# Optimization experiments

Measured on AMD Instinct MI355X. Metric: run time of the kernel, lower is better.

Reference implementation:

```python
import jax, jax.numpy as jnp
import numpy as np

IN_DIM = 128
MEM_DIM = 256
NUM_CLASSES = 12
NUM_LEVELS = 17  # complete binary tree, N = 2**17 - 1 = 131071 nodes


def setup_inputs() -> dict:
    key = jax.random.key(0)
    ks = jax.random.split(key, 7)
    N = 2 ** NUM_LEVELS - 1
    s = 1.0 / np.sqrt(MEM_DIM)  # PyTorch LSTMCell/Linear init scale
    return {
        "x": jax.random.normal(ks[0], (N, IN_DIM), dtype=jnp.float32),
        "W_ih": jax.random.uniform(ks[1], (4 * MEM_DIM, IN_DIM), jnp.float32, -s, s),
        "b_ih": jax.random.uniform(ks[2], (4 * MEM_DIM,), jnp.float32, -s, s),
        "W_hh": jax.random.uniform(ks[3], (4 * MEM_DIM, MEM_DIM), jnp.float32, -s, s),
        "b_hh": jax.random.uniform(ks[4], (4 * MEM_DIM,), jnp.float32, -s, s),
        "W_fc": jax.random.uniform(ks[5], (NUM_CLASSES, MEM_DIM), jnp.float32, -s, s),
        "b_fc": jax.random.uniform(ks[6], (NUM_CLASSES,), jnp.float32, -s, s),
        "num_levels": NUM_LEVELS,
    }


def reference(x, W_ih, b_ih, W_hh, b_hh, W_fc, b_fc, num_levels):
    # Complete binary tree in BFS order: level l occupies nodes [2^l-1, 2^(l+1)-2];
    # children of level-l nodes are exactly the (contiguous) level-(l+1) nodes.
    mem = W_hh.shape[1]
    h_below = None
    c_below = None
    for l in reversed(range(num_levels)):
        n = 2 ** l
        x_l = x[n - 1:2 * n - 1]  # [n, in_dim] nodes at this level
        if h_below is None:  # leaves: zero child state
            ch_h = jnp.zeros((n, mem), dtype=x.dtype)
            ch_c = ch_h
        else:  # sum the two children's (h, c), as the recursion accumulates
            ch_h = h_below.reshape(n, 2, mem).sum(axis=1)
            ch_c = c_below.reshape(n, 2, mem).sum(axis=1)
        # PyTorch LSTMCell: gates = x W_ih^T + b_ih + h W_hh^T + b_hh, chunks i,f,g,o
        gates = x_l @ W_ih.T + b_ih + ch_h @ W_hh.T + b_hh  # [n, 4*mem]
        i, f, g, o = jnp.split(gates, 4, axis=-1)
        c_new = jax.nn.sigmoid(f) * ch_c + jax.nn.sigmoid(i) * jnp.tanh(g)
        h_new = jax.nn.sigmoid(o) * jnp.tanh(c_new)
        h_below, c_below = h_new, c_new
    # Original applies FC to state[1] == cell state c of the root (kept faithfully).
    return c_below[:1] @ W_fc.T + b_fc  # [1, num_classes]
```

## Files before the change

kernel.cpp:

```cpp
#include <hip/hip_runtime.h>
#include <hip/hip_bf16.h>
#include <cstddef>

#define IN_DIM 128
#define MEM 256
#define KTOT 384
#define NLEAF 65536
#define NBLK_TAIL 8

typedef float f32x4 __attribute__((ext_vector_type(4)));
typedef short s16x8 __attribute__((ext_vector_type(8)));
typedef unsigned int u32;

__device__ inline unsigned short f2bf(float f){
    unsigned int u = __builtin_bit_cast(unsigned int, f);
    u += 0x7fff + ((u >> 16) & 1);
    return (unsigned short)(u >> 16);
}

__device__ inline void gld_lds16(const void* g, void* l){
    __builtin_amdgcn_global_load_lds((const __attribute__((address_space(1))) u32*)g,
                                     (__attribute__((address_space(3))) u32*)l, 16, 0, 0);
}
__device__ inline void gld_lds16_dev(const void* g, void* l){
    __builtin_amdgcn_global_load_lds((const __attribute__((address_space(1))) u32*)g,
                                     (__attribute__((address_space(3))) u32*)l, 16, 0, 17);
}
__device__ inline void st16_dev(unsigned short* p, unsigned short v){
    unsigned int vv = v;
    asm volatile("global_store_short %0, %1, off sc0 sc1" :: "v"(p), "v"(vv) : "memory");
}
__device__ inline void st32_dev(float* p, float v){
    asm volatile("global_store_dword %0, %1, off sc0 sc1" :: "v"(p), "v"(v) : "memory");
}

__device__ inline float fsigm(float x){
    return __builtin_amdgcn_rcpf(1.f + __expf(-x));
}
__device__ inline float ftanh(float x){
    return 2.f * __builtin_amdgcn_rcpf(1.f + __expf(-2.f * x)) - 1.f;
}

__host__ __device__ inline size_t offA(int l){
    if (l == 16) return 0;
    return 8388608u + 384u * (65536u - (1u << (l + 1)));
}
#define ARENA_ELEMS 33554048u
#define ARENA_PAD   65536u

__device__ inline void grid_barrier_nf(unsigned* ctr, unsigned target){
    asm volatile("s_waitcnt vmcnt(0)" ::: "memory");
    __syncthreads();
    if (threadIdx.x == 0){
        __hip_atomic_fetch_add(ctr, 1u, __ATOMIC_RELAXED, __HIP_MEMORY_SCOPE_AGENT);
        while (__hip_atomic_load(ctr, __ATOMIC_RELAXED, __HIP_MEMORY_SCOPE_AGENT) < target)
            __builtin_amdgcn_s_sleep(2);
    }
    __syncthreads();
}

__global__ void pack_kernel(const float* __restrict__ x,
                            const float* __restrict__ W_ih, const float* __restrict__ b_ih,
                            const float* __restrict__ W_hh, const float* __restrict__ b_hh,
                            unsigned short* __restrict__ Wp, float* __restrict__ bp,
                            unsigned short* __restrict__ Aarena, unsigned* __restrict__ ctr){
    const int stride = gridDim.x * blockDim.x;
    const int tid0 = blockIdx.x * blockDim.x + threadIdx.x;
    if (tid0 == 0){ ctr[0] = 0; }

    for (int g = tid0; g < 1024 * 48; g += stride){
        int row = g / 48, ko = (g - row * 48) * 8;
        const float* s = (ko < IN_DIM) ? (W_ih + (size_t)row * IN_DIM + ko)
                                       : (W_hh + (size_t)row * MEM + (ko - IN_DIM));
        f32x4 v0 = *(const f32x4*)s, v1 = *(const f32x4*)(s + 4);
        s16x8 o;
        #pragma unroll
        for (int e = 0; e < 4; ++e){ o[e] = (short)f2bf(v0[e]); o[4+e] = (short)f2bf(v1[e]); }
        *(s16x8*)(Wp + (size_t)row * KTOT + ko) = o;
        if (ko == 0) bp[row] = b_ih[row] + b_hh[row];
    }

    const int TOTAL_G = 65536 * 16;
    for (int g = tid0; g < TOTAL_G; g += stride){
        int j  = g >> 4;
        int ko = (g & 15) * 8;
        const f32x4* s = (const f32x4*)(x + (size_t)(65535 + j) * IN_DIM + ko);
        f32x4 v0 = s[0], v1 = s[1];
        s16x8 o;
        #pragma unroll
        for (int e = 0; e < 4; ++e){ o[e] = (short)f2bf(v0[e]); o[4+e] = (short)f2bf(v1[e]); }
        *(s16x8*)(Aarena + (size_t)j * IN_DIM + ko) = o;
    }
}

template<int NK, bool PACKX>
__global__ __launch_bounds__(512, 1) void gemm_lstm8p_kernel(
    const unsigned short* __restrict__ A, int n,
    const unsigned short* __restrict__ Wp, const float* __restrict__ bp,
    const float* __restrict__ csum_in,
    unsigned short* __restrict__ A_next, float* __restrict__ csum_out,
    const float* __restrict__ xsrc, unsigned short* __restrict__ arena)
{
    __shared__ __align__(16) unsigned short As[2][2][128 * 64];
    __shared__ __align__(16) unsigned short Bs[2][2][128 * 64];

    const int tid  = threadIdx.x;
    const int lane = tid & 63;
    const int wid  = tid >> 6;
    const int wm   = wid >> 2;
    const int wn   = wid & 3;
    const int row0 = blockIdx.x * 256;
    const int m0   = blockIdx.y * 64;
    const int mg   = m0 + wn * 16 + (lane & 15);

    auto stageA = [&](int kt, int h){
        #pragma unroll
        for (int i = 0; i < 2; ++i){
            int p  = i * 512 + tid;
            int r  = p >> 3;
            int ls = (p & 7) ^ (r & 7);
            gld_lds16(A + (size_t)(row0 + h * 128 + r) * NK + kt * 64 + ls * 8,
                      (char*)As[kt & 1][h] + (size_t)(i * 512 + wid * 64) * 16);
        }
    };
    auto stageB = [&](int kt, int h){
        #pragma unroll
        for (int i = 0; i < 2; ++i){
            int p  = i * 512 + tid;
            int r  = p >> 3;
            int b  = h * 128 + r;
            int grow = (b >> 6) * 256 + m0 + (b & 63);
            int ls = (p & 7) ^ (r & 7);
            gld_lds16(Wp + (size_t)grow * KTOT + kt * 64 + ls * 8,
                      (char*)Bs[kt & 1][h] + (size_t)(i * 512 + wid * 64) * 16);
        }
    };

    f32x4 acc[8][4];
    #pragma unroll
    for (int r = 0; r < 8; ++r)
        #pragma unroll
        for (int q = 0; q < 4; ++q)
            acc[r][q] = (f32x4){0.f, 0.f, 0.f, 0.f};

    constexpr int nkt = NK / 64;
    stageA(0, 0); stageA(0, 1); stageB(0, 0);
    if (nkt > 1) stageB(1, 0);
    stageB(0, 1);

    s16x8 bfr[2][2];

    #pragma unroll
    for (int t = 0; t < nkt; ++t){
        const unsigned short* Ab = As[t & 1][wm];
        const unsigned short* Bb0 = Bs[t & 1][0];
        const unsigned short* Bb1 = Bs[t & 1][1];

        if (t + 1 < nkt) { asm volatile("s_waitcnt vmcnt(4)" ::: "memory"); }
        else             { asm volatile("s_waitcnt vmcnt(2)" ::: "memory"); }
        __builtin_amdgcn_s_barrier();
        asm volatile("" ::: "memory");

        #pragma unroll
        for (int rh = 0; rh < 2; ++rh){
            s16x8 a[4][2];
            #pragma unroll
            for (int j = 0; j < 4; ++j)
                #pragma unroll
                for (int ks = 0; ks < 2; ++ks){
                    int kb = (((ks * 4 + (lane >> 4)) ^ (lane & 7))) * 8;
                    a[j][ks] = *(const s16x8*)(Ab + (size_t)(rh * 64 + j * 16 + (lane & 15)) * 64 + kb);
                }
            if (rh == 0){
                #pragma unroll
                for (int q2 = 0; q2 < 2; ++q2)
                    #pragma unroll
                    for (int ks = 0; ks < 2; ++ks){
                        int kb = (((ks * 4 + (lane >> 4)) ^ (lane & 7))) * 8;
                        bfr[q2][ks] = *(const s16x8*)(Bb0 + (size_t)(q2 * 64 + wn * 16 + (lane & 15)) * 64 + kb);
                    }
                if (t + 1 < nkt) stageA(t + 1, 0);
            } else {
                if (t + 1 < nkt) stageA(t + 1, 1);
            }
            __builtin_amdgcn_s_setprio(1);
            #pragma unroll
            for (int j = 0; j < 4; ++j)
                #pragma unroll
                for (int q2 = 0; q2 < 2; ++q2)
                    #pragma unroll
                    for (int ks = 0; ks < 2; ++ks)
                        acc[rh * 4 + j][q2] = __builtin_amdgcn_mfma_f32_16x16x32_bf16(
                            a[j][ks], bfr[q2][ks], acc[rh * 4 + j][q2], 0, 0, 0);
            __builtin_amdgcn_s_setprio(0);
        }

        if (t + 1 < nkt) { asm volatile("s_waitcnt vmcnt(4)" ::: "memory"); }
        else             { asm volatile("s_waitcnt vmcnt(0)" ::: "memory"); }
        __builtin_amdgcn_s_barrier();
        asm volatile("" ::: "memory");

        #pragma unroll
        for (int rh = 0; rh < 2; ++rh){
            s16x8 a[4][2];
            #pragma unroll
            for (int j = 0; j < 4; ++j)
                #pragma unroll
                for (int ks = 0; ks < 2; ++ks){
                    int kb = (((ks * 4 + (lane >> 4)) ^ (lane & 7))) * 8;
                    a[j][ks] = *(const s16x8*)(Ab + (size_t)(rh * 64 + j * 16 + (lane & 15)) * 64 + kb);
                }
            if (rh == 0){
                #pragma unroll
                for (int q2 = 0; q2 < 2; ++q2)
                    #pragma unroll
                    for (int ks = 0; ks < 2; ++ks){
                        int kb = (((ks * 4 + (lane >> 4)) ^ (lane & 7))) * 8;
                        bfr[q2][ks] = *(const s16x8*)(Bb1 + (size_t)(q2 * 64 + wn * 16 + (lane & 15)) * 64 + kb);
                    }
                if (t + 2 < nkt) stageB(t + 2, 0);
            } else {
                if (t + 1 < nkt) stageB(t + 1, 1);
            }
            __builtin_amdgcn_s_setprio(1);
            #pragma unroll
            for (int j = 0; j < 4; ++j)
                #pragma unroll
                for (int q2 = 0; q2 < 2; ++q2)
                    #pragma unroll
                    for (int ks = 0; ks < 2; ++ks)
                        acc[rh * 4 + j][2 + q2] = __builtin_amdgcn_mfma_f32_16x16x32_bf16(
                            a[j][ks], bfr[q2][ks], acc[rh * 4 + j][2 + q2], 0, 0, 0);
            __builtin_amdgcn_s_setprio(0);
        }
        __builtin_amdgcn_s_barrier();
        asm volatile("" ::: "memory");
    }

    const float b0 = bp[0 * 256 + mg];
    const float b1 = bp[1 * 256 + mg];
    const float b2 = bp[2 * 256 + mg];
    const float b3 = bp[3 * 256 + mg];
    #pragma unroll
    for (int r = 0; r < 8; ++r){
        const int base = row0 + wm * 128 + r * 16 + (lane >> 4) * 4;
        float cpre[4];
        #pragma unroll
        for (int e = 0; e < 4; ++e)
            cpre[e] = csum_in[(size_t)(base + e) * MEM + mg];
        float cn[4], hn[4];
        #pragma unroll
        for (int e = 0; e < 4; ++e){
            float iv = acc[r][0][e] + b0;
            float fv = acc[r][1][e] + b1;
            float gv = acc[r][2][e] + b2;
            float ov = acc[r][3][e] + b3;
            float c  = fsigm(fv) * cpre[e] + fsigm(iv) * ftanh(gv);
            cn[e] = c;
            hn[e] = fsigm(ov) * ftanh(c);
        }
        int p0 = base >> 1;
        A_next[(size_t)p0 * KTOT + IN_DIM + mg] = f2bf(hn[0] + hn[1]);
        csum_out[(size_t)p0 * MEM + mg] = cn[0] + cn[1];
        A_next[(size_t)(p0 + 1) * KTOT + IN_DIM + mg] = f2bf(hn[2] + hn[3]);
        csum_out[(size_t)(p0 + 1) * MEM + mg] = cn[2] + cn[3];
    }

    if constexpr (PACKX){
        const int TG = 32767 * 16;
        const int bid = blockIdx.y * gridDim.x + blockIdx.x;
        const int stride_g = gridDim.x * gridDim.y * 512;
        for (int g = bid * 512 + tid; g < TG; g += stride_g){
            int i  = g >> 4;
            int ko = (g & 15) * 8;
            int l  = 31 - __clz(i + 1);
            int j  = i + 1 - (1 << l);
            size_t dst = offA(l) + (size_t)j * KTOT + ko;
            const f32x4* s = (const f32x4*)(xsrc + (size_t)i * IN_DIM + ko);
            f32x4 v0 = s[0], v1 = s[1];
            s16x8 o;
            #pragma unroll
            for (int e = 0; e < 4; ++e){ o[e] = (short)f2bf(v0[e]); o[4+e] = (short)f2bf(v1[e]); }
            *(s16x8*)(arena + dst) = o;
        }
    }
}

#define KC 64

template<int NK, int RB, bool LEAF, bool PACKX>
__global__ __launch_bounds__(256) void gemm_lstm_kernel(
    const unsigned short* __restrict__ A, int n,
    const unsigned short* __restrict__ Wp, const float* __restrict__ bp,
    const float* __restrict__ csum_in,
    unsigned short* __restrict__ A_next, float* __restrict__ csum_out,
    const float* __restrict__ xsrc, unsigned short* __restrict__ arena)
{
    constexpr int BM = RB * 32;
    __shared__ __align__(16) unsigned short As[2][BM * KC];
    __shared__ __align__(16) unsigned short Bs[2][128 * KC];

    const int tid  = threadIdx.x;
    const int lane = tid & 63;
    const int wid  = tid >> 6;
    const int wm   = wid >> 1;
    const int wc   = wid & 1;
    const int row0 = blockIdx.x * BM;
    const int m0   = blockIdx.y * 32;

    const int srow = lane >> 3;
    const int scol = ((lane & 7) ^ srow) * 8;

    const int mg = m0 + wc * 16 + (lane & 15);

    const float b0 = bp[0 * 256 + mg];
    const float b1 = LEAF ? 0.f : bp[1 * 256 + mg];
    const float b2 = bp[2 * 256 + mg];
    const float b3 = bp[3 * 256 + mg];
    float cpre[RB][4];
    if (!LEAF){
        #pragma unroll
        for (int r = 0; r < RB; ++r){
            const int base = row0 + wm * (RB * 16) + r * 16 + (lane >> 4) * 4;
            #pragma unroll
            for (int e = 0; e < 4; ++e)
                cpre[r][e] = csum_in[(size_t)(base + e) * MEM + mg];
        }
    }

    f32x4 acc[RB][4];
    #pragma unroll
    for (int r = 0; r < RB; ++r)
        #pragma unroll
        for (int q = 0; q < 4; ++q)
            acc[r][q] = (f32x4){0.f, 0.f, 0.f, 0.f};

    auto stage = [&](int d, int kk){
        char* asb = (char*)As[d];
        char* bsb = (char*)Bs[d];
        #pragma unroll
        for (int q = 0; q < RB; ++q){
            int t = wid * RB + q;
            int r = t * 8 + srow;
            gld_lds16(A + (size_t)(row0 + r) * NK + kk + scol, asb + t * 1024);
        }
        #pragma unroll
        for (int q = 0; q < 4; ++q){
            int t = wid * 4 + q;
            int b = t * 8 + srow;
            int grow = (b >> 5) * 256 + m0 + (b & 31);
            gld_lds16(Wp + (size_t)grow * KTOT + kk + scol, bsb + t * 1024);
        }
    };

    constexpr int nIter = NK / KC;
    stage(0, 0);
    int buf = 0;
    #pragma unroll
    for (int it = 0; it < nIter; ++it){
        if (it + 1 < nIter){
            stage(buf ^ 1, (it + 1) * KC);
            if constexpr (RB == 4) asm volatile("s_waitcnt vmcnt(8)" ::: "memory");
            else                   asm volatile("s_waitcnt vmcnt(6)" ::: "memory");
        } else {
            asm volatile("s_waitcnt vmcnt(0)" ::: "memory");
        }
        __builtin_amdgcn_s_barrier();
        const unsigned short* Ab = As[buf];
        const unsigned short* Bb = Bs[buf];
        #pragma unroll
        for (int ks = 0; ks < 2; ++ks){
            const int slot = ks * 4 + (lane >> 4);
            const int kb = (slot ^ (lane & 7)) * 8;
            s16x8 a[RB], b[4];
            #pragma unroll
            for (int r = 0; r < RB; ++r)
                a[r] = *(const s16x8*)(Ab + (wm * (RB * 16) + r * 16 + (lane & 15)) * KC + kb);
            #pragma unroll
            for (int q = 0; q < 4; ++q)
                b[q] = *(const s16x8*)(Bb + (q * 32 + wc * 16 + (lane & 15)) * KC + kb);
            #pragma unroll
            for (int r = 0; r < RB; ++r)
                #pragma unroll
                for (int q = 0; q < 4; ++q)
                    acc[r][q] = __builtin_amdgcn_mfma_f32_16x16x32_bf16(a[r], b[q], acc[r][q], 0, 0, 0);
        }
        __builtin_amdgcn_s_barrier();
        buf ^= 1;
    }

    #pragma unroll
    for (int r = 0; r < RB; ++r){
        const int base = row0 + wm * (RB * 16) + r * 16 + (lane >> 4) * 4;
        float cn[4], hn[4];
        #pragma unroll
        for (int e = 0; e < 4; ++e){
            float iv = acc[r][0][e] + b0;
            float gv = acc[r][2][e] + b2;
            float ov = acc[r][3][e] + b3;
            float c;
            if (LEAF){
                c = fsigm(iv) * ftanh(gv);
            } else {
                float fv = acc[r][1][e] + b1;
                c = fsigm(fv) * cpre[r][e] + fsigm(iv) * ftanh(gv);
            }
            cn[e] = c;
            hn[e] = fsigm(ov) * ftanh(c);
        }
        if (base < n){
            int p0 = base >> 1;
            A_next[(size_t)p0 * KTOT + IN_DIM + mg] = f2bf(hn[0] + hn[1]);
            csum_out[(size_t)p0 * MEM + mg] = cn[0] + cn[1];
        }
        if (base + 2 < n){
            int p1 = (base >> 1) + 1;
            A_next[(size_t)p1 * KTOT + IN_DIM + mg] = f2bf(hn[2] + hn[3]);
            csum_out[(size_t)p1 * MEM + mg] = cn[2] + cn[3];
        }
    }

    if constexpr (PACKX){
        const int TG = 32768 * 16;
        const int bid = blockIdx.y * gridDim.x + blockIdx.x;
        const int stride_g = gridDim.x * gridDim.y * 256;
        for (int g = bid * 256 + tid; g < TG; g += stride_g){
            int i  = 32767 + (g >> 4);
            int ko = (g & 15) * 8;
            size_t dst = offA(15) + (size_t)(i - 32767) * KTOT + ko;
            const f32x4* s = (const f32x4*)(xsrc + (size_t)i * IN_DIM + ko);
            f32x4 v0 = s[0], v1 = s[1];
            s16x8 o;
            #pragma unroll
            for (int e = 0; e < 4; ++e){ o[e] = (short)f2bf(v0[e]); o[4+e] = (short)f2bf(v1[e]); }
            *(s16x8*)(arena + dst) = o;
        }
    }
}

__global__ __launch_bounds__(512) void tail_kernel(
    const unsigned short* __restrict__ arena,
    const unsigned short* __restrict__ Wp, const float* __restrict__ bp,
    float* cs_in, float* cs_out,
    float* __restrict__ c_root,
    const float* __restrict__ W_fc, const float* __restrict__ b_fc,
    float* __restrict__ out, unsigned* __restrict__ ctr)
{
    __shared__ __align__(16) unsigned short WpL[128 * KTOT];
    __shared__ __align__(16) unsigned short AL[64 * KTOT];

    const int tid  = threadIdx.x;
    const int lane = tid & 63;
    const int wid  = tid >> 6;
    const int wm   = wid >> 1;
    const int wc   = wid & 1;
    const int m0   = blockIdx.x * 32;
    const int mg   = m0 + wc * 16 + (lane & 15);

    #pragma unroll
    for (int i = 0; i < 12; ++i){
        int p0 = wid * 768 + i * 64;
        int p  = p0 + lane;
        int lrow  = p / 48;
        int pslot = p % 48;
        int lslot = pslot ^ (lrow & 7);
        int grow  = (lrow >> 5) * 256 + m0 + (lrow & 31);
        gld_lds16(Wp + (size_t)grow * KTOT + lslot * 8, (char*)WpL + (size_t)p0 * 16);
    }

    const float b0 = bp[0 * 256 + mg];
    const float b1 = bp[1 * 256 + mg];
    const float b2 = bp[2 * 256 + mg];
    const float b3 = bp[3 * 256 + mg];

    asm volatile("s_waitcnt vmcnt(0)" ::: "memory");
    __builtin_amdgcn_s_barrier();

    unsigned gen = 0;
    for (int l = 7; l >= 0; --l){
        const int n = 1 << l;
        const unsigned short* Al = arena + offA(l);
        const int nhalf = (n > 64) ? (n >> 6) : 1;

        for (int h = 0; h < nhalf; ++h){
            const int r0 = h * 64;
            const int rows = (n < 64) ? n : 64;

            const int nslots = rows * 48;
            for (int t = 0; t * 512 < nslots; ++t){
                int pbase = t * 512 + wid * 64;
                int p = pbase + lane;
                if (p < nslots){
                    int row   = p / 48;
                    int pslot = p - row * 48;
                    int lslot = pslot ^ (row & 7);
                    gld_lds16_dev(Al + (size_t)(r0 + row) * KTOT + lslot * 8,
                                  (char*)AL + (size_t)pbase * 16);
                }
            }

            const int base = r0 + wm * 16 + (lane >> 4) * 4;
            float cpre[4];
            #pragma unroll
            for (int e = 0; e < 4; ++e)
                cpre[e] = __hip_atomic_load(&cs_in[(size_t)(base + e) * MEM + mg],
                                            __ATOMIC_RELAXED, __HIP_MEMORY_SCOPE_AGENT);

            asm volatile("s_waitcnt vmcnt(0)" ::: "memory");
            __builtin_amdgcn_s_barrier();

            f32x4 acc[4];
            #pragma unroll
            for (int q = 0; q < 4; ++q)
                acc[q] = (f32x4){0.f, 0.f, 0.f, 0.f};

            #pragma unroll
            for (int kc = 0; kc < 12; ++kc){
                const int ls = kc * 4 + (lane >> 4);
                const int kb = (ls ^ (lane & 7)) * 8;
                s16x8 a = *(const s16x8*)(AL + (size_t)(wm * 16 + (lane & 15)) * KTOT + kb);
                s16x8 b[4];
                #pragma unroll
                for (int q = 0; q < 4; ++q)
                    b[q] = *(const s16x8*)(WpL + (q * 32 + wc * 16 + (lane & 15)) * KTOT + kb);
                #pragma unroll
                for (int q = 0; q < 4; ++q)
                    acc[q] = __builtin_amdgcn_mfma_f32_16x16x32_bf16(a, b[q], acc[q], 0, 0, 0);
            }

            {
                float cn[4], hn[4];
                #pragma unroll
                for (int e = 0; e < 4; ++e){
                    float iv = acc[0][e] + b0;
                    float fv = acc[1][e] + b1;
                    float gv = acc[2][e] + b2;
                    float ov = acc[3][e] + b3;
                    float c  = fsigm(fv) * cpre[e] + fsigm(iv) * ftanh(gv);
                    cn[e] = c;
                    hn[e] = fsigm(ov) * ftanh(c);
                }
                if (l == 0){
                    if (base == 0) st32_dev(&c_root[mg], cn[0]);
                } else {
                    unsigned short* A_next = (unsigned short*)arena + offA(l - 1);
                    if (base < n){
                        int p0 = base >> 1;
                        st16_dev(&A_next[(size_t)p0 * KTOT + IN_DIM + mg], f2bf(hn[0] + hn[1]));
                        st32_dev(&cs_out[(size_t)p0 * MEM + mg], cn[0] + cn[1]);
                    }
                    if (base + 2 < n){
                        int p1 = (base >> 1) + 1;
                        st16_dev(&A_next[(size_t)p1 * KTOT + IN_DIM + mg], f2bf(hn[2] + hn[3]));
                        st32_dev(&cs_out[(size_t)p1 * MEM + mg], cn[2] + cn[3]);
                    }
                }
            }
            __builtin_amdgcn_s_barrier();
        }

        float* t = cs_in; cs_in = cs_out; cs_out = t;
        ++gen;
        grid_barrier_nf(ctr, (unsigned)(NBLK_TAIL * gen));
    }

    if (blockIdx.x == 0 && wid < 4){
        int w = wid;
        for (int cls = w * 3; cls < w * 3 + 3; ++cls){
            float s = 0.f;
            for (int m = lane; m < 256; m += 64){
                float cr = __hip_atomic_load(&c_root[m], __ATOMIC_RELAXED, __HIP_MEMORY_SCOPE_AGENT);
                s += cr * W_fc[cls * 256 + m];
            }
            #pragma unroll
            for (int off = 32; off; off >>= 1)
                s += __shfl_down(s, off, 64);
            if (lane == 0) out[cls] = s + b_fc[cls];
        }
    }
}

extern "C" void kernel_launch(void* const* d_in, const int* in_sizes, int n_in,
                              void* d_out, int out_size, void* d_ws, size_t ws_size,
                              hipStream_t stream)
{
    const float* x    = (const float*)d_in[0];
    const float* W_ih = (const float*)d_in[1];
    const float* b_ih = (const float*)d_in[2];
    const float* W_hh = (const float*)d_in[3];
    const float* b_hh = (const float*)d_in[4];
    const float* W_fc = (const float*)d_in[5];
    const float* b_fc = (const float*)d_in[6];
    float* out = (float*)d_out;

    const size_t OFF_WP = 0;
    const size_t OFF_BP = 786432;
    const size_t OFF_A  = 790528;
    const size_t OFF_CS0 = OFF_A + (size_t)(ARENA_ELEMS + ARENA_PAD) * 2;
    const size_t OFF_CS1 = OFF_CS0 + 33554432;
    const size_t OFF_CR  = OFF_CS1 + 33554432;
    const size_t OFF_CTR = OFF_CR + 1024;
    const size_t NEEDED  = OFF_CTR + 64;
    if (ws_size < NEEDED) return;

    char* ws = (char*)d_ws;
    unsigned short* Wp    = (unsigned short*)(ws + OFF_WP);
    float* bp             = (float*)(ws + OFF_BP);
    unsigned short* arena = (unsigned short*)(ws + OFF_A);
    float* cs0            = (float*)(ws + OFF_CS0);
    float* cs1            = (float*)(ws + OFF_CS1);
    float* c_root         = (float*)(ws + OFF_CR);
    unsigned* ctr         = (unsigned*)(ws + OFF_CTR);

    pack_kernel<<<dim3(2048), dim3(256), 0, stream>>>(
        x, W_ih, b_ih, W_hh, b_hh, Wp, bp, arena, ctr);

    gemm_lstm_kernel<IN_DIM, 4, true, true><<<dim3(NLEAF / 128, 8), dim3(256), 0, stream>>>(
        arena + offA(16), NLEAF, Wp, bp,
        nullptr, arena + offA(15), cs0, x, arena);

    gemm_lstm8p_kernel<KTOT, true><<<dim3(128, 4), dim3(512), 0, stream>>>(
        arena + offA(15), 32768, Wp, bp, cs0, arena + offA(14), cs1, x, arena);
    gemm_lstm8p_kernel<KTOT, false><<<dim3(64, 4), dim3(512), 0, stream>>>(
        arena + offA(14), 16384, Wp, bp, cs1, arena + offA(13), cs0, nullptr, nullptr);

    gemm_lstm_kernel<KTOT, 4, false, false><<<dim3(64, 8), dim3(256), 0, stream>>>(
        arena + offA(13), 8192, Wp, bp, cs0, arena + offA(12), cs1, nullptr, nullptr);

    float* cs_in = cs1; float* cs_out = cs0;
    for (int l = 12; l >= 8; --l){
        int n = 1 << l;
        gemm_lstm_kernel<KTOT, 2, false, false><<<dim3(n / 64, 8), dim3(256), 0, stream>>>(
            arena + offA(l), n, Wp, bp,
            cs_in, arena + offA(l - 1), cs_out, nullptr, nullptr);
        float* t = cs_in; cs_in = cs_out; cs_out = t;
    }

    tail_kernel<<<dim3(NBLK_TAIL), dim3(512), 0, stream>>>(
        arena, Wp, bp, cs_in, cs_out, c_root, W_fc, b_fc, out, ctr);
}
```

Before: 193.3 us.

## Finish small tree levels on a single block to skip grid barriers

The tail kernel now runs only levels 7 and 6 across all tail blocks with grid barriers. Levels 5 down to 0 are computed by block 0 alone, which reads the weights directly from global memory and covers all 256 output columns by giving each wave 32 columns, synchronising with __syncthreads. This removes six grid-wide barriers on the tiny top levels. In exchange, one block does the full-width GEMM for those levels while streaming the weights from global or cache rather than from LDS.

Measured after the change: 355.1 us. +83.7%, slower.

```diff
diff --git a/kernel.cpp b/kernel.cpp
--- a/kernel.cpp
+++ b/kernel.cpp
@@ -477,14 +477,14 @@
     __builtin_amdgcn_s_barrier();
 
     unsigned gen = 0;
-    for (int l = 7; l >= 0; --l){
+    for (int l = 7; l >= 6; --l){
         const int n = 1 << l;
         const unsigned short* Al = arena + offA(l);
         const int nhalf = (n > 64) ? (n >> 6) : 1;
 
         for (int h = 0; h < nhalf; ++h){
             const int r0 = h * 64;
-            const int rows = (n < 64) ? n : 64;
+            const int rows = 64;
 
             const int nslots = rows * 48;
             for (int t = 0; t * 512 < nslots; ++t){
@@ -540,31 +540,147 @@
                     cn[e] = c;
                     hn[e] = fsigm(ov) * ftanh(c);
                 }
+                unsigned short* A_next = (unsigned short*)arena + offA(l - 1);
+                if (base < n){
+                    int p0 = base >> 1;
+                    st16_dev(&A_next[(size_t)p0 * KTOT + IN_DIM + mg], f2bf(hn[0] + hn[1]));
+                    st32_dev(&cs_out[(size_t)p0 * MEM + mg], cn[0] + cn[1]);
+                }
+                if (base + 2 < n){
+                    int p1 = (base >> 1) + 1;
+                    st16_dev(&A_next[(size_t)p1 * KTOT + IN_DIM + mg], f2bf(hn[2] + hn[3]));
+                    st32_dev(&cs_out[(size_t)p1 * MEM + mg], cn[2] + cn[3]);
+                }
+            }
+            __builtin_amdgcn_s_barrier();
+        }
+
+        float* t = cs_in; cs_in = cs_out; cs_out = t;
+        ++gen;
+        grid_barrier_nf(ctr, (unsigned)(NBLK_TAIL * gen));
+    }
+
+    if (blockIdx.x != 0) return;
+
+    for (int l = 5; l >= 0; --l){
+        const int n = 1 << l;
+        const unsigned short* Al = arena + offA(l);
+
+        const int nslots = n * 48;
+        {
+            int pbase = wid * 64;
+            int p = pbase + lane;
+            for (int t = 0; t * 512 < nslots; ++t){
+                int pb = t * 512 + pbase;
+                int pp = t * 512 + p;
+                if (pp < nslots){
+                    int row   = pp / 48;
+                    int pslot = pp - row * 48;
+                    int lslot = pslot ^ (row & 7);
+                    gld_lds16_dev(Al + (size_t)row * KTOT + lslot * 8,
+                                  (char*)AL + (size_t)pb * 16);
+                }
+            }
+        }
+
+        float cpre[2][2][4];
+        #pragma unroll
+        for (int rf = 0; rf < 2; ++rf){
+            #pragma unroll
+            for (int cg = 0; cg < 2; ++cg){
+                const int base = rf * 16 + (lane >> 4) * 4;
+                const int mgx  = wid * 32 + cg * 16 + (lane & 15);
+                #pragma unroll
+                for (int e = 0; e < 4; ++e)
+                    cpre[rf][cg][e] = __hip_atomic_load(&cs_in[(size_t)(base + e) * MEM + mgx],
+                                                        __ATOMIC_RELAXED, __HIP_MEMORY_SCOPE_AGENT);
+            }
+        }
+
+        asm volatile("s_waitcnt vmcnt(0)" ::: "memory");
+        __syncthreads();
+
+        f32x4 acc[2][2][4];
+        #pragma unroll
+        for (int rf = 0; rf < 2; ++rf)
+            #pragma unroll
+            for (int cg = 0; cg < 2; ++cg)
+                #pragma unroll
+                for (int g = 0; g < 4; ++g)
+                    acc[rf][cg][g] = (f32x4){0.f, 0.f, 0.f, 0.f};
+
+        const int nrf = (n > 16) ? 2 : 1;
+        #pragma unroll
+        for (int kc = 0; kc < 12; ++kc){
+            const int ls = kc * 4 + (lane >> 4);
+            const int kb = (ls ^ (lane & 7)) * 8;
+            const int kk = ls * 8;
+            s16x8 a[2];
+            a[0] = *(const s16x8*)(AL + (size_t)(lane & 15) * KTOT + kb);
+            if (nrf > 1)
+                a[1] = *(const s16x8*)(AL + (size_t)(16 + (lane & 15)) * KTOT + kb);
+            s16x8 b[2][4];
+            #pragma unroll
+            for (int cg = 0; cg < 2; ++cg)
+                #pragma unroll
+                for (int g = 0; g < 4; ++g)
+                    b[cg][g] = *(const s16x8*)(Wp + (size_t)(g * 256 + wid * 32 + cg * 16 + (lane & 15)) * KTOT + kk);
+            #pragma unroll
+            for (int cg = 0; cg < 2; ++cg)
+                #pragma unroll
+                for (int g = 0; g < 4; ++g){
+                    acc[0][cg][g] = __builtin_amdgcn_mfma_f32_16x16x32_bf16(a[0], b[cg][g], acc[0][cg][g], 0, 0, 0);
+                    if (nrf > 1)
+                        acc[1][cg][g] = __builtin_amdgcn_mfma_f32_16x16x32_bf16(a[1], b[cg][g], acc[1][cg][g], 0, 0, 0);
+                }
+        }
+
+        #pragma unroll
+        for (int rf = 0; rf < 2; ++rf){
+            if (rf >= nrf) break;
+            #pragma unroll
+            for (int cg = 0; cg < 2; ++cg){
+                const int base = rf * 16 + (lane >> 4) * 4;
+                const int mgx  = wid * 32 + cg * 16 + (lane & 15);
+                const float bb0 = bp[0 * 256 + mgx];
+                const float bb1 = bp[1 * 256 + mgx];
+                const float bb2 = bp[2 * 256 + mgx];
+                const float bb3 = bp[3 * 256 + mgx];
+                float cn[4], hn[4];
+                #pragma unroll
+                for (int e = 0; e < 4; ++e){
+                    float iv = acc[rf][cg][0][e] + bb0;
+                    float fv = acc[rf][cg][1][e] + bb1;
+                    float gv = acc[rf][cg][2][e] + bb2;
+                    float ov = acc[rf][cg][3][e] + bb3;
+                    float c  = fsigm(fv) * cpre[rf][cg][e] + fsigm(iv) * ftanh(gv);
+                    cn[e] = c;
+                    hn[e] = fsigm(ov) * ftanh(c);
+                }
                 if (l == 0){
-                    if (base == 0) st32_dev(&c_root[mg], cn[0]);
+                    if (base == 0) st32_dev(&c_root[mgx], cn[0]);
                 } else {
                     unsigned short* A_next = (unsigned short*)arena + offA(l - 1);
                     if (base < n){
                         int p0 = base >> 1;
-                        st16_dev(&A_next[(size_t)p0 * KTOT + IN_DIM + mg], f2bf(hn[0] + hn[1]));
-                        st32_dev(&cs_out[(size_t)p0 * MEM + mg], cn[0] + cn[1]);
+                        st16_dev(&A_next[(size_t)p0 * KTOT + IN_DIM + mgx], f2bf(hn[0] + hn[1]));
+                        st32_dev(&cs_out[(size_t)p0 * MEM + mgx], cn[0] + cn[1]);
                     }
                     if (base + 2 < n){
                         int p1 = (base >> 1) + 1;
-                        st16_dev(&A_next[(size_t)p1 * KTOT + IN_DIM + mg], f2bf(hn[2] + hn[3]));
-                        st32_dev(&cs_out[(size_t)p1 * MEM + mg], cn[2] + cn[3]);
+                        st16_dev(&A_next[(size_t)p1 * KTOT + IN_DIM + mgx], f2bf(hn[2] + hn[3]));
+                        st32_dev(&cs_out[(size_t)p1 * MEM + mgx], cn[2] + cn[3]);
                     }
                 }
             }
-            __builtin_amdgcn_s_barrier();
         }
 
         float* t = cs_in; cs_in = cs_out; cs_out = t;
-        ++gen;
-        grid_barrier_nf(ctr, (unsigned)(NBLK_TAIL * gen));
-    }
-
-    if (blockIdx.x == 0 && wid < 4){
+        asm volatile("s_waitcnt vmcnt(0)" ::: "memory");
+        __syncthreads();
+    }
+
+    if (wid < 4){
         int w = wid;
         for (int cls = w * 3; cls < w * 3 + 3; ++cls){
             float s = 0.f;
```
